# Kernel optimization log

Measured on AMD Instinct MI355X. Metric: run time of the kernel, lower is better.

Reference implementation:

```python
import jax, jax.numpy as jnp
import numpy as np

B, TI, TO = 32, 128, 64
VI, VO = 32000, 32000
E, H, A = 256, 512, 512
EOS, BOS = 0, 1


def setup_inputs() -> dict:
    key = jax.random.key(0)
    ks = jax.random.split(key, 24)
    def p(k, shape):
        return jax.random.normal(k, shape, jnp.float32) * 0.05
    return {
        "inp": jax.random.randint(ks[0], (B, TI), 0, VI),
        "out": jax.random.randint(ks[1], (B, TO), 0, VO),
        "emb_inp": p(ks[2], (VI, E)),
        "emb_out": p(ks[3], (VO, E)),
        "enc_Wih_f": p(ks[4], (3 * H, E)),
        "enc_Whh_f": p(ks[5], (3 * H, H)),
        "enc_bih_f": p(ks[6], (3 * H,)),
        "enc_bhh_f": p(ks[7], (3 * H,)),
        "enc_Wih_b": p(ks[8], (3 * H, E)),
        "enc_Whh_b": p(ks[9], (3 * H, H)),
        "enc_bih_b": p(ks[10], (3 * H,)),
        "enc_bhh_b": p(ks[11], (3 * H,)),
        "dec_start_W": p(ks[12], (H, 2 * H)),
        "dec_start_b": p(ks[13], (H,)),
        "dec_Wih": p(ks[14], (3 * H, E + 2 * H)),
        "dec_Whh": p(ks[15], (3 * H, H)),
        "dec_bih": p(ks[16], (3 * H,)),
        "dec_bhh": p(ks[17], (3 * H,)),
        "attn_Wenc": p(ks[18], (A, 2 * H)),
        "attn_benc": p(ks[19], (A,)),
        "attn_Wdec": p(ks[20], (A, H)),
        "attn_bdec": p(ks[21], (A,)),
        "attn_v": p(ks[22], (A,)),
        "attn_vb": jnp.zeros((), jnp.float32),
        "logits_W": p(ks[23], (VO, 3 * H)),
        "logits_b": jnp.zeros((VO,), jnp.float32),
    }


def _gru_dir(x, Wih, bih, Whh, bhh, reverse):
    # x: [B,T,E]; precompute input projections once: [B,T,3H]
    xp = jnp.einsum('bte,ge->btg', x, Wih) + bih
    Hd = Whh.shape[1]
    def step(h, xt):
        gh = h @ Whh.T + bhh
        xr, xz, xn = jnp.split(xt, 3, -1)
        hr, hz, hn = jnp.split(gh, 3, -1)
        r = jax.nn.sigmoid(xr + hr)
        z = jax.nn.sigmoid(xz + hz)
        n = jnp.tanh(xn + r * hn)
        h_new = (1.0 - z) * n + z * h
        return h_new, h_new
    h0 = jnp.zeros((x.shape[0], Hd), x.dtype)
    _, hs = jax.lax.scan(step, h0, jnp.swapaxes(xp, 0, 1), reverse=reverse)
    return jnp.swapaxes(hs, 0, 1)  # [B,T,H]


def _forward(inp, out, emb_inp, emb_out,
             enc_Wih_f, enc_Whh_f, enc_bih_f, enc_bhh_f,
             enc_Wih_b, enc_Whh_b, enc_bih_b, enc_bhh_b,
             dec_start_W, dec_start_b, dec_Wih, dec_Whh, dec_bih, dec_bhh,
             attn_Wenc, attn_benc, attn_Wdec, attn_bdec, attn_v, attn_vb,
             logits_W, logits_b):
    x = emb_inp[inp]  # [B,TI,E]
    ef = _gru_dir(x, enc_Wih_f, enc_bih_f, enc_Whh_f, enc_bhh_f, False)
    eb = _gru_dir(x, enc_Wih_b, enc_bih_b, enc_Whh_b, enc_bhh_b, True)
    enc = jnp.concatenate([ef, eb], -1)  # [B,TI,2H]
    mask = (inp != EOS).astype(jnp.float32)
    lengths = jnp.minimum(mask.sum(1).astype(jnp.int32), TI - 1)
    last = enc[jnp.arange(enc.shape[0]), lengths]  # [B,2H]
    dec0 = last @ dec_start_W.T + dec_start_b  # [B,H]
    enc_proj = jnp.einsum('btd,ad->bta', enc, attn_Wenc) + attn_benc  # [B,TI,A]

    def attend(dec):
        dp = dec @ attn_Wdec.T + attn_bdec  # [B,A]
        s = jnp.tanh(enc_proj + dp[:, None, :]) @ attn_v + attn_vb  # [B,TI]
        s = jnp.where(mask > 0, s, -jnp.inf)
        pr = jax.nn.softmax(s, -1)
        return jnp.einsum('bt,btd->bd', pr, enc), pr

    a0, _ = attend(dec0)

    def step(carry, tok):
        h, a = carry
        e = emb_out[tok]  # [B,E]
        xg = jnp.concatenate([e, a], -1) @ dec_Wih.T + dec_bih
        hg = h @ dec_Whh.T + dec_bhh
        xr, xz, xn = jnp.split(xg, 3, -1)
        hr, hz, hn = jnp.split(hg, 3, -1)
        r = jax.nn.sigmoid(xr + hr)
        z = jax.nn.sigmoid(xz + hz)
        n = jnp.tanh(xn + r * hn)
        h_new = (1.0 - z) * n + z * h
        a_new, _ = attend(h_new)
        lg = jnp.concatenate([h_new, a_new], -1) @ logits_W.T + logits_b
        return (h_new, a_new), lg

    toks = jnp.swapaxes(out[:, :-1], 0, 1)  # [TO-1, B]
    _, lgs = jax.lax.scan(step, (dec0, a0), toks)  # [TO-1,B,VO]
    first = jnp.log(jax.nn.one_hot(jnp.full((out.shape[0],), BOS), VO) + 1e-9)
    return jnp.swapaxes(jnp.concatenate([first[None], lgs], 0), 0, 1)  # [B,TO,VO]


def reference(inp, out, emb_inp, emb_out,
              enc_Wih_f, enc_Whh_f, enc_bih_f, enc_bhh_f,
              enc_Wih_b, enc_Whh_b, enc_bih_b, enc_bhh_b,
              dec_start_W, dec_start_b, dec_Wih, dec_Whh, dec_bih, dec_bhh,
              attn_Wenc, attn_benc, attn_Wdec, attn_bdec, attn_v, attn_vb,
              logits_W, logits_b):
    return _forward(inp, out, emb_inp, emb_out,
                    enc_Wih_f, enc_Whh_f, enc_bih_f, enc_bhh_f,
                    enc_Wih_b, enc_Whh_b, enc_bih_b, enc_bhh_b,
                    dec_start_W, dec_start_b, dec_Wih, dec_Whh, dec_bih, dec_bhh,
                    attn_Wenc, attn_benc, attn_Wdec, attn_bdec, attn_v, attn_vb,
                    logits_W, logits_b)
```

## Files before the change

### kernel.cpp

```cpp
#include <hip/hip_runtime.h>
#include <math.h>
#include <stdint.h>

#define B_   32
#define TI_  128
#define TO_  64
#define E_   256
#define H_   512
#define A_   512
#define VO_  32000
#define G3_  1536
#define D2H_ 1024

using short8 = __attribute__((ext_vector_type(8))) short;
using f32x4  = __attribute__((ext_vector_type(4))) float;

__device__ __forceinline__ unsigned short f2bf(float x) {
  uint32_t u = __builtin_bit_cast(uint32_t, x);
  uint32_t r = (u + 0x7fffu + ((u >> 16) & 1u)) >> 16;
  return (unsigned short)r;
}


__global__ __launch_bounds__(256) void k_zero(float* __restrict__ p, int n) {
  int i = blockIdx.x * 256 + threadIdx.x;
  if (i < n) p[i] = 0.f;
}

__global__ __launch_bounds__(256) void k_zero_u16(unsigned short* __restrict__ p, int n) {
  int i = blockIdx.x * 256 + threadIdx.x;
  if (i < n) p[i] = 0;
}

__global__ __launch_bounds__(256) void k_cvt_bf16(const float* __restrict__ in,
                                                  unsigned short* __restrict__ out, int n8) {
  int i = blockIdx.x * 256 + threadIdx.x;
  if (i >= n8) return;
  float4 a = ((const float4*)in)[2 * i];
  float4 b = ((const float4*)in)[2 * i + 1];
  ushort4 lo = make_ushort4(f2bf(a.x), f2bf(a.y), f2bf(a.z), f2bf(a.w));
  ushort4 hi = make_ushort4(f2bf(b.x), f2bf(b.y), f2bf(b.z), f2bf(b.w));
  ((ushort4*)out)[2 * i] = lo;
  ((ushort4*)out)[2 * i + 1] = hi;
}

__global__ __launch_bounds__(256) void k_gather_x(const int* __restrict__ inp,
                                                  const float* __restrict__ emb,
                                                  float* __restrict__ x) {
  int idx = blockIdx.x * 256 + threadIdx.x;
  int total = B_ * TI_ * E_ / 4;
  if (idx >= total) return;
  int row = idx / (E_ / 4);
  int e4  = idx % (E_ / 4);
  int tok = inp[row];
  ((float4*)x)[idx] = ((const float4*)emb)[(size_t)tok * (E_ / 4) + e4];
}

__global__ __launch_bounds__(256) void k_gather_xe(const int* __restrict__ outidx,
                                                   const float* __restrict__ emb,
                                                   float* __restrict__ xe) {
  int idx = blockIdx.x * 256 + threadIdx.x;
  int total = 63 * B_ * E_ / 4;
  if (idx >= total) return;
  int row = idx / (E_ / 4);
  int e4  = idx % (E_ / 4);
  int i = row / B_, b = row % B_;
  int tok = outidx[b * TO_ + i];
  ((float4*)xe)[idx] = ((const float4*)emb)[(size_t)tok * (E_ / 4) + e4];
}

__global__ __launch_bounds__(256) void k_first(float* __restrict__ dout) {
  int idx = blockIdx.x * 256 + threadIdx.x;
  if (idx >= B_ * VO_) return;
  int b = idx / VO_, v = idx % VO_;
  dout[(size_t)b * TO_ * VO_ + v] = (v == 1) ? 0.f : -20.72326583694641f;
}


__global__ __launch_bounds__(256) void k_gemm128(
    const float* __restrict__ A, int lda,
    const float* __restrict__ W, int ldw,
    const float* __restrict__ bias,
    float* __restrict__ C, int M, int N, int K) {
  __shared__ float As[32][132];
  __shared__ float Bs[32][132];
  const int tid = threadIdx.x;
  const int m0 = blockIdx.y * 128, n0 = blockIdx.x * 128;
  const int tx = tid & 15, ty = tid >> 4;
  float acc[8][8];
#pragma unroll
  for (int i = 0; i < 8; ++i)
#pragma unroll
    for (int j = 0; j < 8; ++j) acc[i][j] = 0.f;

  for (int k0 = 0; k0 < K; k0 += 32) {
#pragma unroll
    for (int i = 0; i < 16; ++i) {
      int idx = tid + i * 256;
      int kk = idx & 31, mm = idx >> 5;
      int m = m0 + mm;
      As[kk][mm] = (m < M) ? A[(size_t)m * lda + k0 + kk] : 0.f;
      Bs[kk][mm] = W[(size_t)(n0 + mm) * ldw + k0 + kk];
    }
    __syncthreads();
#pragma unroll
    for (int kk = 0; kk < 32; ++kk) {
      float4 a0 = *(const float4*)&As[kk][ty * 8];
      float4 a1 = *(const float4*)&As[kk][ty * 8 + 4];
      float4 b0 = *(const float4*)&Bs[kk][tx * 8];
      float4 b1 = *(const float4*)&Bs[kk][tx * 8 + 4];
      float av[8] = {a0.x, a0.y, a0.z, a0.w, a1.x, a1.y, a1.z, a1.w};
      float bv[8] = {b0.x, b0.y, b0.z, b0.w, b1.x, b1.y, b1.z, b1.w};
#pragma unroll
      for (int i = 0; i < 8; ++i)
#pragma unroll
        for (int j = 0; j < 8; ++j) acc[i][j] = fmaf(av[i], bv[j], acc[i][j]);
    }
    __syncthreads();
  }

#pragma unroll
  for (int i = 0; i < 8; ++i) {
    int m = m0 + ty * 8 + i;
    if (m >= M) continue;
#pragma unroll
    for (int j = 0; j < 8; ++j) {
      int n = n0 + tx * 8 + j;
      C[(size_t)m * N + n] = acc[i][j] + bias[n];
    }
  }
}


__global__ __launch_bounds__(256) void k_logits_mfma(
    const unsigned short* __restrict__ A,
    const unsigned short* __restrict__ Bt,
    const float* __restrict__ bias,
    float* __restrict__ out) {
  __shared__ alignas(16) unsigned short As[128 * 32];
  __shared__ alignas(16) unsigned short Bs[128 * 32];
  const int tid = threadIdx.x;
  const int wave = tid >> 6, lane = tid & 63;
  const int m0 = blockIdx.y * 128, n0 = blockIdx.x * 128;
  const int wr = wave >> 1, wc = wave & 1;
  const int K = G3_;

  f32x4 acc[4][4];
#pragma unroll
  for (int i = 0; i < 4; ++i)
#pragma unroll
    for (int j = 0; j < 4; ++j) acc[i][j] = (f32x4){0.f, 0.f, 0.f, 0.f};

  const int srow = tid >> 2;
  const int sbyte = (tid & 3) * 16;
  const int fr = lane & 15;
  const int fkb = (lane >> 4) * 16;

  for (int k0 = 0; k0 < K; k0 += 32) {
#pragma unroll
    for (int rd = 0; rd < 2; ++rd) {
      int row = rd * 64 + srow;
      const char* ga = (const char*)(A + (size_t)(m0 + row) * K + k0) + sbyte;
      const char* gb = (const char*)(Bt + (size_t)(n0 + row) * K + k0) + sbyte;
      __builtin_amdgcn_global_load_lds(
          (const __attribute__((address_space(1))) uint32_t*)ga,
          (__attribute__((address_space(3))) uint32_t*)((char*)As + rd * 4096 + wave * 1024),
          16, 0, 0);
      __builtin_amdgcn_global_load_lds(
          (const __attribute__((address_space(1))) uint32_t*)gb,
          (__attribute__((address_space(3))) uint32_t*)((char*)Bs + rd * 4096 + wave * 1024),
          16, 0, 0);
    }
    __syncthreads();

    short8 af[4], bf[4];
#pragma unroll
    for (int i = 0; i < 4; ++i) {
      int ar = wr * 64 + i * 16 + fr;
      int bc = wc * 64 + i * 16 + fr;
      af[i] = *(const short8*)((const char*)As + ar * 64 + fkb);
      bf[i] = *(const short8*)((const char*)Bs + bc * 64 + fkb);
    }
#pragma unroll
    for (int i = 0; i < 4; ++i)
#pragma unroll
      for (int j = 0; j < 4; ++j)
        acc[i][j] = __builtin_amdgcn_mfma_f32_16x16x32_bf16(af[i], bf[j], acc[i][j], 0, 0, 0);
    __syncthreads();
  }

  const int crow = (lane >> 4) * 4, ccol = lane & 15;
#pragma unroll
  for (int i = 0; i < 4; ++i) {
#pragma unroll
    for (int r = 0; r < 4; ++r) {
      int m = m0 + wr * 64 + i * 16 + crow + r;
      if (m >= 63 * B_) continue;
      int b = m & 31, st = m >> 5;
      float* orow = out + ((size_t)b * TO_ + st + 1) * VO_;
#pragma unroll
      for (int j = 0; j < 4; ++j) {
        int n = n0 + wc * 64 + j * 16 + ccol;
        orow[n] = acc[i][j][r] + bias[n];
      }
    }
  }
}


__global__ __launch_bounds__(256) void k_enc_step(
    const float* __restrict__ hf_in, float* __restrict__ hf_out,
    const float* __restrict__ hb_in, float* __restrict__ hb_out,
    const float* __restrict__ xp_f, const float* __restrict__ xp_b,
    const float* __restrict__ Whh_f, const float* __restrict__ bhh_f,
    const float* __restrict__ Whh_b, const float* __restrict__ bhh_b,
    float* __restrict__ enc, int t) {
  __shared__ float hs[32 * 516];
  const int bid = blockIdx.x;
  const int dir = bid >> 6;
  const int slice = bid & 63;
  const float* h_in  = dir ? hb_in : hf_in;
  float*       h_out = dir ? hb_out : hf_out;
  const float* xp    = dir ? xp_b : xp_f;
  const float* Whh   = dir ? Whh_b : Whh_f;
  const float* bhh   = dir ? bhh_b : bhh_f;
  const int tt = dir ? (TI_ - 1 - t) : t;
  const int tid = threadIdx.x;

#pragma unroll
  for (int i = 0; i < 16; ++i) {
    int idx4 = tid + i * 256;
    int flat = idx4 * 4;
    int mm = flat >> 9, kk = flat & 511;
    *(float4*)&hs[mm * 516 + kk] = *(const float4*)(h_in + (size_t)mm * H_ + kk);
  }
  __syncthreads();

  const int m = tid & 31, c = tid >> 5;
  const int col = slice * 8 + c;
  const float* hrow = hs + m * 516;
  const float4* wr = (const float4*)(Whh + (size_t)col * H_);
  const float4* wz = (const float4*)(Whh + (size_t)(H_ + col) * H_);
  const float4* wn = (const float4*)(Whh + (size_t)(2 * H_ + col) * H_);
  float accr = 0.f, accz = 0.f, accn = 0.f;
#pragma unroll 4
  for (int k4 = 0; k4 < H_ / 4; ++k4) {
    float4 h4 = *(const float4*)(hrow + k4 * 4);
    float4 r = wr[k4], z = wz[k4], n = wn[k4];
    accr = fmaf(h4.x, r.x, fmaf(h4.y, r.y, fmaf(h4.z, r.z, fmaf(h4.w, r.w, accr))));
    accz = fmaf(h4.x, z.x, fmaf(h4.y, z.y, fmaf(h4.z, z.z, fmaf(h4.w, z.w, accz))));
    accn = fmaf(h4.x, n.x, fmaf(h4.y, n.y, fmaf(h4.z, n.z, fmaf(h4.w, n.w, accn))));
  }
  size_t xoff = ((size_t)m * TI_ + tt) * G3_ + col;
  float xr = xp[xoff], xz = xp[xoff + 512], xn = xp[xoff + 1024];
  float hr = accr + bhh[col];
  float hz = accz + bhh[512 + col];
  float hn = accn + bhh[1024 + col];
  float r = 1.f / (1.f + expf(-(xr + hr)));
  float z = 1.f / (1.f + expf(-(xz + hz)));
  float nn = tanhf(xn + r * hn);
  float hold = hrow[col];
  float hnew = (1.f - z) * nn + z * hold;
  h_out[m * H_ + col] = hnew;
  enc[((size_t)m * TI_ + tt) * D2H_ + dir * H_ + col] = hnew;
}


__global__ __launch_bounds__(256) void k_dec_step(
    const float* __restrict__ h_in, float* __restrict__ h_out,
    const float* __restrict__ a_in, const float* __restrict__ XE,
    const float* __restrict__ Wih, const float* __restrict__ Whh,
    const float* __restrict__ bhh,
    unsigned short* __restrict__ HA, int step) {
  __shared__ float buf[32 * 516];
  const int tid = threadIdx.x;
  const int m = tid & 31, c = tid >> 5;
  const int col = blockIdx.x * 8 + c;
  const float* hrow = buf + m * 516;
  float axr = 0.f, axz = 0.f, axn = 0.f, ahr = 0.f, ahz = 0.f, ahn = 0.f;

#pragma unroll
  for (int i = 0; i < 16; ++i) {
    int idx4 = tid + i * 256;
    int flat = idx4 * 4;
    int mm = flat >> 9, kk = flat & 511;
    *(float4*)&buf[mm * 516 + kk] = *(const float4*)(a_in + (size_t)mm * D2H_ + kk);
  }
  __syncthreads();
  {
    const float4* wr = (const float4*)(Wih + (size_t)col * 1280 + 256);
    const float4* wz = (const float4*)(Wih + (size_t)(512 + col) * 1280 + 256);
    const float4* wn = (const float4*)(Wih + (size_t)(1024 + col) * 1280 + 256);
#pragma unroll 4
    for (int k4 = 0; k4 < 128; ++k4) {
      float4 h4 = *(const float4*)(hrow + k4 * 4);
      float4 r = wr[k4], z = wz[k4], n = wn[k4];
      axr = fmaf(h4.x, r.x, fmaf(h4.y, r.y, fmaf(h4.z, r.z, fmaf(h4.w, r.w, axr))));
      axz = fmaf(h4.x, z.x, fmaf(h4.y, z.y, fmaf(h4.z, z.z, fmaf(h4.w, z.w, axz))));
      axn = fmaf(h4.x, n.x, fmaf(h4.y, n.y, fmaf(h4.z, n.z, fmaf(h4.w, n.w, axn))));
    }
  }
  __syncthreads();

#pragma unroll
  for (int i = 0; i < 16; ++i) {
    int idx4 = tid + i * 256;
    int flat = idx4 * 4;
    int mm = flat >> 9, kk = flat & 511;
    *(float4*)&buf[mm * 516 + kk] = *(const float4*)(a_in + (size_t)mm * D2H_ + 512 + kk);
  }
  __syncthreads();
  {
    const float4* wr = (const float4*)(Wih + (size_t)col * 1280 + 768);
    const float4* wz = (const float4*)(Wih + (size_t)(512 + col) * 1280 + 768);
    const float4* wn = (const float4*)(Wih + (size_t)(1024 + col) * 1280 + 768);
#pragma unroll 4
    for (int k4 = 0; k4 < 128; ++k4) {
      float4 h4 = *(const float4*)(hrow + k4 * 4);
      float4 r = wr[k4], z = wz[k4], n = wn[k4];
      axr = fmaf(h4.x, r.x, fmaf(h4.y, r.y, fmaf(h4.z, r.z, fmaf(h4.w, r.w, axr))));
      axz = fmaf(h4.x, z.x, fmaf(h4.y, z.y, fmaf(h4.z, z.z, fmaf(h4.w, z.w, axz))));
      axn = fmaf(h4.x, n.x, fmaf(h4.y, n.y, fmaf(h4.z, n.z, fmaf(h4.w, n.w, axn))));
    }
  }
  __syncthreads();

#pragma unroll
  for (int i = 0; i < 16; ++i) {
    int idx4 = tid + i * 256;
    int flat = idx4 * 4;
    int mm = flat >> 9, kk = flat & 511;
    *(float4*)&buf[mm * 516 + kk] = *(const float4*)(h_in + (size_t)mm * H_ + kk);
  }
  __syncthreads();
  {
    const float4* wr = (const float4*)(Whh + (size_t)col * H_);
    const float4* wz = (const float4*)(Whh + (size_t)(512 + col) * H_);
    const float4* wn = (const float4*)(Whh + (size_t)(1024 + col) * H_);
#pragma unroll 4
    for (int k4 = 0; k4 < 128; ++k4) {
      float4 h4 = *(const float4*)(hrow + k4 * 4);
      float4 r = wr[k4], z = wz[k4], n = wn[k4];
      ahr = fmaf(h4.x, r.x, fmaf(h4.y, r.y, fmaf(h4.z, r.z, fmaf(h4.w, r.w, ahr))));
      ahz = fmaf(h4.x, z.x, fmaf(h4.y, z.z, fmaf(h4.z, z.z, fmaf(h4.w, z.w, ahz))));
      ahn = fmaf(h4.x, n.x, fmaf(h4.y, n.y, fmaf(h4.z, n.z, fmaf(h4.w, n.w, ahn))));
    }
  }

  size_t xrow = ((size_t)step * B_ + m) * G3_;
  float xr = XE[xrow + col] + axr;
  float xz = XE[xrow + 512 + col] + axz;
  float xn = XE[xrow + 1024 + col] + axn;
  float hr = ahr + bhh[col];
  float hz = ahz + bhh[512 + col];
  float hn = ahn + bhh[1024 + col];
  float r = 1.f / (1.f + expf(-(xr + hr)));
  float z = 1.f / (1.f + expf(-(xz + hz)));
  float nn = tanhf(xn + r * hn);
  float hold = hrow[col];
  float hnew = (1.f - z) * nn + z * hold;
  h_out[m * H_ + col] = hnew;
  HA[xrow + col] = f2bf(hnew);
}


__global__ __launch_bounds__(256) void k_attend(
    const float* __restrict__ h_src, const float* __restrict__ enc,
    const float* __restrict__ enc_proj, const int* __restrict__ inp,
    const float* __restrict__ Wdec, const float* __restrict__ bdec,
    const float* __restrict__ v, const float* __restrict__ vb,
    float* __restrict__ a_out, unsigned short* __restrict__ HA, int step) {
  __shared__ float hq[512];
  __shared__ float dp[512];
  __shared__ float vv[512];
  __shared__ float part[256];
  __shared__ float sc[128];
  __shared__ float red[128];
  const int b = blockIdx.x, tid = threadIdx.x;

  hq[tid] = h_src[b * H_ + tid];
  hq[tid + 256] = h_src[b * H_ + 256 + tid];
  vv[tid] = v[tid];
  vv[tid + 256] = v[tid + 256];
  __syncthreads();

#pragma unroll
  for (int jj = 0; jj < 2; ++jj) {
    int j = tid + jj * 256;
    const float4* w4 = (const float4*)(Wdec + (size_t)j * H_);
    float acc = 0.f;
#pragma unroll 4
    for (int k4 = 0; k4 < H_ / 4; ++k4) {
      float4 w = w4[k4];
      float4 h4 = *(const float4*)&hq[k4 * 4];
      acc = fmaf(h4.x, w.x, fmaf(h4.y, w.y, fmaf(h4.z, w.z, fmaf(h4.w, w.w, acc))));
    }
    dp[j] = acc + bdec[j];
  }
  __syncthreads();

  {
    int t = tid & 127, half = tid >> 7;
    const float* ep = enc_proj + ((size_t)b * TI_ + t) * A_ + half * 256;
    const float* dph = dp + half * 256;
    const float* vh = vv + half * 256;
    float p = 0.f;
    for (int a = 0; a < 256; ++a) p = fmaf(vh[a], tanhf(ep[a] + dph[a]), p);
    part[tid] = p;
  }
  __syncthreads();
  if (tid < 128) {
    float s = part[tid] + part[tid + 128] + vb[0];
    if (inp[b * TI_ + tid] == 0) s = -INFINITY;
    sc[tid] = s;
    red[tid] = s;
  }
  __syncthreads();
  for (int o = 64; o > 0; o >>= 1) {
    if (tid < o) red[tid] = fmaxf(red[tid], red[tid + o]);
    __syncthreads();
  }
  float mx = red[0];
  __syncthreads();
  if (tid < 128) {
    float e = expf(sc[tid] - mx);
    sc[tid] = e;
    red[tid] = e;
  }
  __syncthreads();
  for (int o = 64; o > 0; o >>= 1) {
    if (tid < o) red[tid] += red[tid + o];
    __syncthreads();
  }
  float inv = 1.f / red[0];
  __syncthreads();

  float4 acc = make_float4(0.f, 0.f, 0.f, 0.f);
  const float4* e4p = (const float4*)(enc + (size_t)b * TI_ * D2H_) + tid;
#pragma unroll 4
  for (int t2 = 0; t2 < TI_; ++t2) {
    float pr = sc[t2] * inv;
    float4 ev = e4p[(size_t)t2 * (D2H_ / 4)];
    acc.x = fmaf(pr, ev.x, acc.x);
    acc.y = fmaf(pr, ev.y, acc.y);
    acc.z = fmaf(pr, ev.z, acc.z);
    acc.w = fmaf(pr, ev.w, acc.w);
  }
  *(float4*)(a_out + (size_t)b * D2H_ + tid * 4) = acc;
  if (step >= 0) {
    unsigned short* hp = HA + ((size_t)step * B_ + b) * G3_ + H_ + tid * 4;
    *(ushort4*)hp = make_ushort4(f2bf(acc.x), f2bf(acc.y), f2bf(acc.z), f2bf(acc.w));
  }
}


__global__ __launch_bounds__(256) void k_dec0(
    const int* __restrict__ inp, const float* __restrict__ enc,
    const float* __restrict__ Wst, const float* __restrict__ bst,
    float* __restrict__ h0) {
  __shared__ float last[1024];
  __shared__ int redi[128];
  __shared__ int slen;
  const int b = blockIdx.x, tid = threadIdx.x;
  if (tid < 128) redi[tid] = (inp[b * TI_ + tid] != 0) ? 1 : 0;
  __syncthreads();
  for (int o = 64; o > 0; o >>= 1) {
    if (tid < o) redi[tid] += redi[tid + o];
    __syncthreads();
  }
  if (tid == 0) slen = min(redi[0], TI_ - 1);
  __syncthreads();
  int len = slen;
#pragma unroll
  for (int i = 0; i < 4; ++i)
    last[tid + i * 256] = enc[((size_t)b * TI_ + len) * D2H_ + tid + i * 256];
  __syncthreads();
#pragma unroll
  for (int jj = 0; jj < 2; ++jj) {
    int j = tid + jj * 256;
    const float4* w4 = (const float4*)(Wst + (size_t)j * D2H_);
    float acc = 0.f;
#pragma unroll 4
    for (int k4 = 0; k4 < D2H_ / 4; ++k4) {
      float4 w = w4[k4];
      float4 l4 = *(const float4*)&last[k4 * 4];
      acc = fmaf(l4.x, w.x, fmaf(l4.y, w.y, fmaf(l4.z, w.z, fmaf(l4.w, w.w, acc))));
    }
    h0[b * H_ + j] = acc + bst[j];
  }
}


extern "C" void kernel_launch(void* const* d_in, const int* in_sizes, int n_in,
                              void* d_out, int out_size, void* d_ws, size_t ws_size,
                              hipStream_t stream) {
  const int*   inp     = (const int*)d_in[0];
  const int*   outi    = (const int*)d_in[1];
  const float* emb_inp = (const float*)d_in[2];
  const float* emb_out = (const float*)d_in[3];
  const float* eWih_f  = (const float*)d_in[4];
  const float* eWhh_f  = (const float*)d_in[5];
  const float* ebih_f  = (const float*)d_in[6];
  const float* ebhh_f  = (const float*)d_in[7];
  const float* eWih_b  = (const float*)d_in[8];
  const float* eWhh_b  = (const float*)d_in[9];
  const float* ebih_b  = (const float*)d_in[10];
  const float* ebhh_b  = (const float*)d_in[11];
  const float* dsW     = (const float*)d_in[12];
  const float* dsb     = (const float*)d_in[13];
  const float* dWih    = (const float*)d_in[14];
  const float* dWhh    = (const float*)d_in[15];
  const float* dbih    = (const float*)d_in[16];
  const float* dbhh    = (const float*)d_in[17];
  const float* aWenc   = (const float*)d_in[18];
  const float* abenc   = (const float*)d_in[19];
  const float* aWdec   = (const float*)d_in[20];
  const float* abdec   = (const float*)d_in[21];
  const float* av      = (const float*)d_in[22];
  const float* avb     = (const float*)d_in[23];
  const float* lW      = (const float*)d_in[24];
  const float* lb      = (const float*)d_in[25];
  float* dout = (float*)d_out;

  float* ws = (float*)d_ws;
  size_t off = 0;
  auto alloc = [&](size_t n) { float* p = ws + off; off += n; return p; };
  float* x    = alloc((size_t)B_ * TI_ * E_);
  float* xp_f = alloc((size_t)B_ * TI_ * G3_);
  float* xp_b = alloc((size_t)B_ * TI_ * G3_);
  float* enc  = alloc((size_t)B_ * TI_ * D2H_);
  float* encp = alloc((size_t)B_ * TI_ * A_);
  float* xe   = alloc((size_t)63 * B_ * E_);
  float* XE   = alloc((size_t)63 * B_ * G3_);
  unsigned short* HAb = (unsigned short*)alloc((size_t)2048 * G3_ / 2);
  unsigned short* lWb = (unsigned short*)alloc((size_t)VO_ * G3_ / 2);
  float* hf0  = alloc(B_ * H_);
  float* hf1  = alloc(B_ * H_);
  float* hb0  = alloc(B_ * H_);
  float* hb1  = alloc(B_ * H_);
  float* hd0  = alloc(B_ * H_);
  float* hd1  = alloc(B_ * H_);
  float* adec = alloc(B_ * D2H_);

  k_zero<<<(2 * B_ * H_ + 255) / 256, 256, 0, stream>>>(hf0, B_ * H_);
  k_zero<<<(2 * B_ * H_ + 255) / 256, 256, 0, stream>>>(hb0, B_ * H_);
  k_zero_u16<<<(32 * G3_) / 256, 256, 0, stream>>>(HAb + (size_t)2016 * G3_, 32 * G3_);

  k_cvt_bf16<<<((VO_ * G3_ / 8) + 255) / 256, 256, 0, stream>>>(lW, lWb, VO_ * G3_ / 8);

  k_gather_x<<<(B_ * TI_ * E_ / 4 + 255) / 256, 256, 0, stream>>>(inp, emb_inp, x);
  dim3 g1(G3_ / 128, (B_ * TI_) / 128);
  k_gemm128<<<g1, 256, 0, stream>>>(x, E_, eWih_f, E_, ebih_f, xp_f, B_ * TI_, G3_, E_);
  k_gemm128<<<g1, 256, 0, stream>>>(x, E_, eWih_b, E_, ebih_b, xp_b, B_ * TI_, G3_, E_);

  float* hfb[2] = {hf0, hf1};
  float* hbb[2] = {hb0, hb1};
  for (int t = 0; t < TI_; ++t) {
    k_enc_step<<<128, 256, 0, stream>>>(hfb[t & 1], hfb[(t + 1) & 1],
                                        hbb[t & 1], hbb[(t + 1) & 1],
                                        xp_f, xp_b, eWhh_f, ebhh_f, eWhh_b, ebhh_b,
                                        enc, t);
  }

  dim3 g2(A_ / 128, (B_ * TI_) / 128);
  k_gemm128<<<g2, 256, 0, stream>>>(enc, D2H_, aWenc, D2H_, abenc, encp, B_ * TI_, A_, D2H_);

  k_dec0<<<B_, 256, 0, stream>>>(inp, enc, dsW, dsb, hd0);
  k_attend<<<B_, 256, 0, stream>>>(hd0, enc, encp, inp, aWdec, abdec, av, avb, adec, HAb, -1);

  k_gather_xe<<<(63 * B_ * E_ / 4 + 255) / 256, 256, 0, stream>>>(outi, emb_out, xe);
  dim3 g3(G3_ / 128, (63 * B_ + 127) / 128);
  k_gemm128<<<g3, 256, 0, stream>>>(xe, E_, dWih, E_ + D2H_, dbih, XE, 63 * B_, G3_, E_);

  float* hdb[2] = {hd0, hd1};
  for (int i = 0; i < 63; ++i) {
    k_dec_step<<<64, 256, 0, stream>>>(hdb[i & 1], hdb[(i + 1) & 1], adec, XE,
                                       dWih, dWhh, dbhh, HAb, i);
    k_attend<<<B_, 256, 0, stream>>>(hdb[(i + 1) & 1], enc, encp, inp,
                                     aWdec, abdec, av, avb, adec, HAb, i);
  }

  dim3 g4(VO_ / 128, 16);
  k_logits_mfma<<<g4, 256, 0, stream>>>(HAb, lWb, lb, dout);

  k_first<<<(B_ * VO_ + 255) / 256, 256, 0, stream>>>(dout);
}
```

Baseline: 10.89 ms.

## Fuse encoder and decoder step loops into persistent kernels with grid barriers

Replaces the 128 per-timestep encoder launches with one persistent 128-block kernel, and the 127 decoder-step and attend launches with one persistent 64-block kernel. Steps inside each kernel are separated by a software grid barrier built from an atomic counter. This removes per-launch overhead and launch gaps on the serial recurrence. In exchange, every block must be co-resident and the spin barrier carries its own latency. The encoder also gains a redundant tanh expression that is computed and then overwritten.

```diff
diff --git a/kernel.cpp b/kernel.cpp
--- a/kernel.cpp
+++ b/kernel.cpp
@@ -21,15 +21,26 @@
   return (unsigned short)r;
 }
 
-
-__global__ __launch_bounds__(256) void k_zero(float* __restrict__ p, int n) {
+__device__ __forceinline__ void gbar(int* bar, int target) {
+  __syncthreads();
+  if (threadIdx.x == 0) {
+    __threadfence();
+    atomicAdd(bar, 1);
+    while (__hip_atomic_load(bar, __ATOMIC_RELAXED, __HIP_MEMORY_SCOPE_AGENT) < target)
+      __builtin_amdgcn_s_sleep(4);
+    __threadfence();
+  }
+  __syncthreads();
+}
+
+__global__ __launch_bounds__(256) void k_init(float* __restrict__ hf0,
+                                              float* __restrict__ hb0,
+                                              unsigned short* __restrict__ HAtail,
+                                              int* __restrict__ bar) {
   int i = blockIdx.x * 256 + threadIdx.x;
-  if (i < n) p[i] = 0.f;
-}
-
-__global__ __launch_bounds__(256) void k_zero_u16(unsigned short* __restrict__ p, int n) {
-  int i = blockIdx.x * 256 + threadIdx.x;
-  if (i < n) p[i] = 0;
+  if (i < B_ * H_) { hf0[i] = 0.f; hb0[i] = 0.f; }
+  if (i < 32 * G3_) HAtail[i] = 0;
+  if (i < 2) bar[i] = 0;
 }
 
 __global__ __launch_bounds__(256) void k_cvt_bf16(const float* __restrict__ in,
@@ -38,10 +49,8 @@
   if (i >= n8) return;
   float4 a = ((const float4*)in)[2 * i];
   float4 b = ((const float4*)in)[2 * i + 1];
-  ushort4 lo = make_ushort4(f2bf(a.x), f2bf(a.y), f2bf(a.z), f2bf(a.w));
-  ushort4 hi = make_ushort4(f2bf(b.x), f2bf(b.y), f2bf(b.z), f2bf(b.w));
-  ((ushort4*)out)[2 * i] = lo;
-  ((ushort4*)out)[2 * i + 1] = hi;
+  ((ushort4*)out)[2 * i]     = make_ushort4(f2bf(a.x), f2bf(a.y), f2bf(a.z), f2bf(a.w));
+  ((ushort4*)out)[2 * i + 1] = make_ushort4(f2bf(b.x), f2bf(b.y), f2bf(b.z), f2bf(b.w));
 }
 
 __global__ __launch_bounds__(256) void k_gather_x(const int* __restrict__ inp,
@@ -76,7 +85,6 @@
   dout[(size_t)b * TO_ * VO_ + v] = (v == 1) ? 0.f : -20.72326583694641f;
 }
 
-
 __global__ __launch_bounds__(256) void k_gemm128(
     const float* __restrict__ A, int lda,
     const float* __restrict__ W, int ldw,
@@ -130,7 +138,6 @@
     }
   }
 }
-
 
 __global__ __launch_bounds__(256) void k_logits_mfma(
     const unsigned short* __restrict__ A,
@@ -208,176 +215,75 @@
 }
 
 
-__global__ __launch_bounds__(256) void k_enc_step(
-    const float* __restrict__ hf_in, float* __restrict__ hf_out,
-    const float* __restrict__ hb_in, float* __restrict__ hb_out,
+__global__ __launch_bounds__(256) void k_encoder(
     const float* __restrict__ xp_f, const float* __restrict__ xp_b,
     const float* __restrict__ Whh_f, const float* __restrict__ bhh_f,
     const float* __restrict__ Whh_b, const float* __restrict__ bhh_b,
-    float* __restrict__ enc, int t) {
+    float* __restrict__ hf0, float* __restrict__ hf1,
+    float* __restrict__ hb0, float* __restrict__ hb1,
+    float* __restrict__ enc, int* __restrict__ bar) {
   __shared__ float hs[32 * 516];
   const int bid = blockIdx.x;
-  const int dir = bid >> 6;
-  const int slice = bid & 63;
-  const float* h_in  = dir ? hb_in : hf_in;
-  float*       h_out = dir ? hb_out : hf_out;
-  const float* xp    = dir ? xp_b : xp_f;
-  const float* Whh   = dir ? Whh_b : Whh_f;
-  const float* bhh   = dir ? bhh_b : bhh_f;
-  const int tt = dir ? (TI_ - 1 - t) : t;
+  const int dir = bid >> 6, slice = bid & 63;
+  const float* xp  = dir ? xp_b : xp_f;
+  const float* Whh = dir ? Whh_b : Whh_f;
+  const float* bhh = dir ? bhh_b : bhh_f;
+  float* hp0 = dir ? hb0 : hf0;
+  float* hp1 = dir ? hb1 : hf1;
   const int tid = threadIdx.x;
-
-#pragma unroll
-  for (int i = 0; i < 16; ++i) {
-    int idx4 = tid + i * 256;
-    int flat = idx4 * 4;
-    int mm = flat >> 9, kk = flat & 511;
-    *(float4*)&hs[mm * 516 + kk] = *(const float4*)(h_in + (size_t)mm * H_ + kk);
-  }
-  __syncthreads();
-
   const int m = tid & 31, c = tid >> 5;
   const int col = slice * 8 + c;
   const float* hrow = hs + m * 516;
   const float4* wr = (const float4*)(Whh + (size_t)col * H_);
   const float4* wz = (const float4*)(Whh + (size_t)(H_ + col) * H_);
   const float4* wn = (const float4*)(Whh + (size_t)(2 * H_ + col) * H_);
-  float accr = 0.f, accz = 0.f, accn = 0.f;
-#pragma unroll 4
-  for (int k4 = 0; k4 < H_ / 4; ++k4) {
-    float4 h4 = *(const float4*)(hrow + k4 * 4);
-    float4 r = wr[k4], z = wz[k4], n = wn[k4];
-    accr = fmaf(h4.x, r.x, fmaf(h4.y, r.y, fmaf(h4.z, r.z, fmaf(h4.w, r.w, accr))));
-    accz = fmaf(h4.x, z.x, fmaf(h4.y, z.y, fmaf(h4.z, z.z, fmaf(h4.w, z.w, accz))));
-    accn = fmaf(h4.x, n.x, fmaf(h4.y, n.y, fmaf(h4.z, n.z, fmaf(h4.w, n.w, accn))));
-  }
-  size_t xoff = ((size_t)m * TI_ + tt) * G3_ + col;
-  float xr = xp[xoff], xz = xp[xoff + 512], xn = xp[xoff + 1024];
-  float hr = accr + bhh[col];
-  float hz = accz + bhh[512 + col];
-  float hn = accn + bhh[1024 + col];
-  float r = 1.f / (1.f + expf(-(xr + hr)));
-  float z = 1.f / (1.f + expf(-(xz + hz)));
-  float nn = tanhf(xn + r * hn);
-  float hold = hrow[col];
-  float hnew = (1.f - z) * nn + z * hold;
-  h_out[m * H_ + col] = hnew;
-  enc[((size_t)m * TI_ + tt) * D2H_ + dir * H_ + col] = hnew;
-}
-
-
-__global__ __launch_bounds__(256) void k_dec_step(
-    const float* __restrict__ h_in, float* __restrict__ h_out,
-    const float* __restrict__ a_in, const float* __restrict__ XE,
-    const float* __restrict__ Wih, const float* __restrict__ Whh,
-    const float* __restrict__ bhh,
-    unsigned short* __restrict__ HA, int step) {
-  __shared__ float buf[32 * 516];
-  const int tid = threadIdx.x;
-  const int m = tid & 31, c = tid >> 5;
-  const int col = blockIdx.x * 8 + c;
-  const float* hrow = buf + m * 516;
-  float axr = 0.f, axz = 0.f, axn = 0.f, ahr = 0.f, ahz = 0.f, ahn = 0.f;
-
-#pragma unroll
-  for (int i = 0; i < 16; ++i) {
-    int idx4 = tid + i * 256;
-    int flat = idx4 * 4;
-    int mm = flat >> 9, kk = flat & 511;
-    *(float4*)&buf[mm * 516 + kk] = *(const float4*)(a_in + (size_t)mm * D2H_ + kk);
-  }
-  __syncthreads();
-  {
-    const float4* wr = (const float4*)(Wih + (size_t)col * 1280 + 256);
-    const float4* wz = (const float4*)(Wih + (size_t)(512 + col) * 1280 + 256);
-    const float4* wn = (const float4*)(Wih + (size_t)(1024 + col) * 1280 + 256);
-#pragma unroll 4
-    for (int k4 = 0; k4 < 128; ++k4) {
+  const float br = bhh[col], bz = bhh[512 + col], bn = bhh[1024 + col];
+
+  for (int t = 0; t < TI_; ++t) {
+    const float* h_in = (t & 1) ? hp1 : hp0;
+    float*       h_out = (t & 1) ? hp0 : hp1;
+    const int tt = dir ? (TI_ - 1 - t) : t;
+
+#pragma unroll
+    for (int i = 0; i < 16; ++i) {
+      int flat = (tid + i * 256) * 4;
+      int mm = flat >> 9, kk = flat & 511;
+      *(float4*)&hs[mm * 516 + kk] = *(const float4*)(h_in + (size_t)mm * H_ + kk);
+    }
+    __syncthreads();
+
+    float accr = 0.f, accz = 0.f, accn = 0.f;
+#pragma unroll 4
+    for (int k4 = 0; k4 < H_ / 4; ++k4) {
       float4 h4 = *(const float4*)(hrow + k4 * 4);
       float4 r = wr[k4], z = wz[k4], n = wn[k4];
-      axr = fmaf(h4.x, r.x, fmaf(h4.y, r.y, fmaf(h4.z, r.z, fmaf(h4.w, r.w, axr))));
-      axz = fmaf(h4.x, z.x, fmaf(h4.y, z.y, fmaf(h4.z, z.z, fmaf(h4.w, z.w, axz))));
-      axn = fmaf(h4.x, n.x, fmaf(h4.y, n.y, fmaf(h4.z, n.z, fmaf(h4.w, n.w, axn))));
-    }
-  }
-  __syncthreads();
-
-#pragma unroll
-  for (int i = 0; i < 16; ++i) {
-    int idx4 = tid + i * 256;
-    int flat = idx4 * 4;
-    int mm = flat >> 9, kk = flat & 511;
-    *(float4*)&buf[mm * 516 + kk] = *(const float4*)(a_in + (size_t)mm * D2H_ + 512 + kk);
-  }
-  __syncthreads();
-  {
-    const float4* wr = (const float4*)(Wih + (size_t)col * 1280 + 768);
-    const float4* wz = (const float4*)(Wih + (size_t)(512 + col) * 1280 + 768);
-    const float4* wn = (const float4*)(Wih + (size_t)(1024 + col) * 1280 + 768);
-#pragma unroll 4
-    for (int k4 = 0; k4 < 128; ++k4) {
-      float4 h4 = *(const float4*)(hrow + k4 * 4);
-      float4 r = wr[k4], z = wz[k4], n = wn[k4];
-      axr = fmaf(h4.x, r.x, fmaf(h4.y, r.y, fmaf(h4.z, r.z, fmaf(h4.w, r.w, axr))));
-      axz = fmaf(h4.x, z.x, fmaf(h4.y, z.y, fmaf(h4.z, z.z, fmaf(h4.w, z.w, axz))));
-      axn = fmaf(h4.x, n.x, fmaf(h4.y, n.y, fmaf(h4.z, n.z, fmaf(h4.w, n.w, axn))));
-    }
-  }
-  __syncthreads();
-
-#pragma unroll
-  for (int i = 0; i < 16; ++i) {
-    int idx4 = tid + i * 256;
-    int flat = idx4 * 4;
-    int mm = flat >> 9, kk = flat & 511;
-    *(float4*)&buf[mm * 516 + kk] = *(const float4*)(h_in + (size_t)mm * H_ + kk);
-  }
-  __syncthreads();
-  {
-    const float4* wr = (const float4*)(Whh + (size_t)col * H_);
-    const float4* wz = (const float4*)(Whh + (size_t)(512 + col) * H_);
-    const float4* wn = (const float4*)(Whh + (size_t)(1024 + col) * H_);
-#pragma unroll 4
-    for (int k4 = 0; k4 < 128; ++k4) {
-      float4 h4 = *(const float4*)(hrow + k4 * 4);
-      float4 r = wr[k4], z = wz[k4], n = wn[k4];
-      ahr = fmaf(h4.x, r.x, fmaf(h4.y, r.y, fmaf(h4.z, r.z, fmaf(h4.w, r.w, ahr))));
-      ahz = fmaf(h4.x, z.x, fmaf(h4.y, z.z, fmaf(h4.z, z.z, fmaf(h4.w, z.w, ahz))));
-      ahn = fmaf(h4.x, n.x, fmaf(h4.y, n.y, fmaf(h4.z, n.z, fmaf(h4.w, n.w, ahn))));
-    }
-  }
-
-  size_t xrow = ((size_t)step * B_ + m) * G3_;
-  float xr = XE[xrow + col] + axr;
-  float xz = XE[xrow + 512 + col] + axz;
-  float xn = XE[xrow + 1024 + col] + axn;
-  float hr = ahr + bhh[col];
-  float hz = ahz + bhh[512 + col];
-  float hn = ahn + bhh[1024 + col];
-  float r = 1.f / (1.f + expf(-(xr + hr)));
-  float z = 1.f / (1.f + expf(-(xz + hz)));
-  float nn = tanhf(xn + r * hn);
-  float hold = hrow[col];
-  float hnew = (1.f - z) * nn + z * hold;
-  h_out[m * H_ + col] = hnew;
-  HA[xrow + col] = f2bf(hnew);
-}
-
-
-__global__ __launch_bounds__(256) void k_attend(
-    const float* __restrict__ h_src, const float* __restrict__ enc,
-    const float* __restrict__ enc_proj, const int* __restrict__ inp,
-    const float* __restrict__ Wdec, const float* __restrict__ bdec,
-    const float* __restrict__ v, const float* __restrict__ vb,
-    float* __restrict__ a_out, unsigned short* __restrict__ HA, int step) {
-  __shared__ float hq[512];
-  __shared__ float dp[512];
-  __shared__ float vv[512];
-  __shared__ float part[256];
-  __shared__ float sc[128];
-  __shared__ float red[128];
-  const int b = blockIdx.x, tid = threadIdx.x;
-
+      accr = fmaf(h4.x, r.x, fmaf(h4.y, r.y, fmaf(h4.z, r.z, fmaf(h4.w, r.w, accr))));
+      accz = fmaf(h4.x, z.x, fmaf(h4.y, z.y, fmaf(h4.z, z.z, fmaf(h4.w, z.w, accz))));
+      accn = fmaf(h4.x, n.x, fmaf(h4.y, n.y, fmaf(h4.z, n.z, fmaf(h4.w, n.w, accn))));
+    }
+    size_t xoff = ((size_t)m * TI_ + tt) * G3_ + col;
+    float xr = xp[xoff], xz = xp[xoff + 512], xn = xp[xoff + 1024];
+    float r = 1.f / (1.f + expf(-(xr + accr + br)));
+    float z = 1.f / (1.f + expf(-(xz + accz + bz)));
+    float nn = tanhf(xn + accn + bn + r * 0.f + r * (accn * 0.f) + r * 0.f + (accn + bn) * 0.f + r * ((accn + bn) - (accn + bn)) + r * (accn + bn) - r * (accn + bn));
+    nn = tanhf(xn + r * (accn + bn));
+    float hold = hrow[col];
+    float hnew = (1.f - z) * nn + z * hold;
+    h_out[m * H_ + col] = hnew;
+    enc[((size_t)m * TI_ + tt) * D2H_ + dir * H_ + col] = hnew;
+
+    if (t < TI_ - 1) gbar(bar, 128 * (t + 1));
+  }
+}
+
+
+__device__ void attend_body(int b, int tid,
+                            const float* __restrict__ h_src, const float* __restrict__ enc,
+                            const float* __restrict__ encp, const int* __restrict__ inp,
+                            const float* __restrict__ Wdec, const float* __restrict__ bdec,
+                            const float* __restrict__ v, const float* __restrict__ vb,
+                            float* __restrict__ a_out, unsigned short* __restrict__ HA, int step,
+                            float* hq, float* dp, float* vv, float* part, float* sc, float* red) {
   hq[tid] = h_src[b * H_ + tid];
   hq[tid + 256] = h_src[b * H_ + 256 + tid];
   vv[tid] = v[tid];
@@ -401,7 +307,7 @@
 
   {
     int t = tid & 127, half = tid >> 7;
-    const float* ep = enc_proj + ((size_t)b * TI_ + t) * A_ + half * 256;
+    const float* ep = encp + ((size_t)b * TI_ + t) * A_ + half * 256;
     const float* dph = dp + half * 256;
     const float* vh = vv + half * 256;
     float p = 0.f;
@@ -453,40 +359,159 @@
   }
 }
 
-
-__global__ __launch_bounds__(256) void k_dec0(
+__device__ void dec_step_body(int bid, int tid,
+                              const float* __restrict__ h_in, float* __restrict__ h_out,
+                              const float* __restrict__ a_in, const float* __restrict__ XE,
+                              const float* __restrict__ Wih, const float* __restrict__ Whh,
+                              const float* __restrict__ bhh,
+                              unsigned short* __restrict__ HA, int step, float* buf) {
+  const int m = tid & 31, c = tid >> 5;
+  const int col = bid * 8 + c;
+  const float* hrow = buf + m * 516;
+  float axr = 0.f, axz = 0.f, axn = 0.f, ahr = 0.f, ahz = 0.f, ahn = 0.f;
+
+#pragma unroll
+  for (int i = 0; i < 16; ++i) {
+    int flat = (tid + i * 256) * 4;
+    int mm = flat >> 9, kk = flat & 511;
+    *(float4*)&buf[mm * 516 + kk] = *(const float4*)(a_in + (size_t)mm * D2H_ + kk);
+  }
+  __syncthreads();
+  {
+    const float4* wr = (const float4*)(Wih + (size_t)col * 1280 + 256);
+    const float4* wz = (const float4*)(Wih + (size_t)(512 + col) * 1280 + 256);
+    const float4* wn = (const float4*)(Wih + (size_t)(1024 + col) * 1280 + 256);
+#pragma unroll 4
+    for (int k4 = 0; k4 < 128; ++k4) {
+      float4 h4 = *(const float4*)(hrow + k4 * 4);
+      float4 r = wr[k4], z = wz[k4], n = wn[k4];
+      axr = fmaf(h4.x, r.x, fmaf(h4.y, r.y, fmaf(h4.z, r.z, fmaf(h4.w, r.w, axr))));
+      axz = fmaf(h4.x, z.x, fmaf(h4.y, z.y, fmaf(h4.z, z.z, fmaf(h4.w, z.w, axz))));
+      axn = fmaf(h4.x, n.x, fmaf(h4.y, n.y, fmaf(h4.z, n.z, fmaf(h4.w, n.w, axn))));
+    }
+  }
+  __syncthreads();
+
+#pragma unroll
+  for (int i = 0; i < 16; ++i) {
+    int flat = (tid + i * 256) * 4;
+    int mm = flat >> 9, kk = flat & 511;
+    *(float4*)&buf[mm * 516 + kk] = *(const float4*)(a_in + (size_t)mm * D2H_ + 512 + kk);
+  }
+  __syncthreads();
+  {
+    const float4* wr = (const float4*)(Wih + (size_t)col * 1280 + 768);
+    const float4* wz = (const float4*)(Wih + (size_t)(512 + col) * 1280 + 768);
+    const float4* wn = (const float4*)(Wih + (size_t)(1024 + col) * 1280 + 768);
+#pragma unroll 4
+    for (int k4 = 0; k4 < 128; ++k4) {
+      float4 h4 = *(const float4*)(hrow + k4 * 4);
+      float4 r = wr[k4], z = wz[k4], n = wn[k4];
+      axr = fmaf(h4.x, r.x, fmaf(h4.y, r.y, fmaf(h4.z, r.z, fmaf(h4.w, r.w, axr))));
+      axz = fmaf(h4.x, z.x, fmaf(h4.y, z.y, fmaf(h4.z, z.z, fmaf(h4.w, z.w, axz))));
+      axn = fmaf(h4.x, n.x, fmaf(h4.y, n.y, fmaf(h4.z, n.z, fmaf(h4.w, n.w, axn))));
+    }
+  }
+  __syncthreads();
+
+#pragma unroll
+  for (int i = 0; i < 16; ++i) {
+    int flat = (tid + i * 256) * 4;
+    int mm = flat >> 9, kk = flat & 511;
+    *(float4*)&buf[mm * 516 + kk] = *(const float4*)(h_in + (size_t)mm * H_ + kk);
+  }
+  __syncthreads();
+  {
+    const float4* wr = (const float4*)(Whh + (size_t)col * H_);
+    const float4* wz = (const float4*)(Whh + (size_t)(512 + col) * H_);
+    const float4* wn = (const float4*)(Whh + (size_t)(1024 + col) * H_);
+#pragma unroll 4
+    for (int k4 = 0; k4 < 128; ++k4) {
+      float4 h4 = *(const float4*)(hrow + k4 * 4);
+      float4 r = wr[k4], z = wz[k4], n = wn[k4];
+      ahr = fmaf(h4.x, r.x, fmaf(h4.y, r.y, fmaf(h4.z, r.z, fmaf(h4.w, r.w, ahr))));
+      ahz = fmaf(h4.x, z.x, fmaf(h4.y, z.y, fmaf(h4.z, z.z, fmaf(h4.w, z.w, ahz))));
+      ahn = fmaf(h4.x, n.x, fmaf(h4.y, n.y, fmaf(h4.z, n.z, fmaf(h4.w, n.w, ahn))));
+    }
+  }
+
+  size_t xrow = ((size_t)step * B_ + m) * G3_;
+  float xr = XE[xrow + col] + axr;
+  float xz = XE[xrow + 512 + col] + axz;
+  float xn = XE[xrow + 1024 + col] + axn;
+  float r = 1.f / (1.f + expf(-(xr + ahr + bhh[col])));
+  float z = 1.f / (1.f + expf(-(xz + ahz + bhh[512 + col])));
+  float nn = tanhf(xn + r * (ahn + bhh[1024 + col]));
+  float hold = hrow[col];
+  float hnew = (1.f - z) * nn + z * hold;
+  h_out[m * H_ + col] = hnew;
+  HA[xrow + col] = f2bf(hnew);
+}
+
+
+__global__ __launch_bounds__(256) void k_decoder(
     const int* __restrict__ inp, const float* __restrict__ enc,
-    const float* __restrict__ Wst, const float* __restrict__ bst,
-    float* __restrict__ h0) {
-  __shared__ float last[1024];
+    const float* __restrict__ encp,
+    const float* __restrict__ dsW, const float* __restrict__ dsb,
+    const float* __restrict__ XE, const float* __restrict__ dWih,
+    const float* __restrict__ dWhh, const float* __restrict__ dbhh,
+    const float* __restrict__ aWdec, const float* __restrict__ abdec,
+    const float* __restrict__ av, const float* __restrict__ avb,
+    float* __restrict__ hd0, float* __restrict__ hd1,
+    float* __restrict__ adec, unsigned short* __restrict__ HAb,
+    int* __restrict__ bar) {
+  __shared__ float buf[32 * 516];
+  __shared__ float hq[512], dp[512], vv[512], part[256], sc[128], red[128];
   __shared__ int redi[128];
   __shared__ int slen;
-  const int b = blockIdx.x, tid = threadIdx.x;
-  if (tid < 128) redi[tid] = (inp[b * TI_ + tid] != 0) ? 1 : 0;
-  __syncthreads();
-  for (int o = 64; o > 0; o >>= 1) {
-    if (tid < o) redi[tid] += redi[tid + o];
-    __syncthreads();
-  }
-  if (tid == 0) slen = min(redi[0], TI_ - 1);
-  __syncthreads();
-  int len = slen;
-#pragma unroll
-  for (int i = 0; i < 4; ++i)
-    last[tid + i * 256] = enc[((size_t)b * TI_ + len) * D2H_ + tid + i * 256];
-  __syncthreads();
-#pragma unroll
-  for (int jj = 0; jj < 2; ++jj) {
-    int j = tid + jj * 256;
-    const float4* w4 = (const float4*)(Wst + (size_t)j * D2H_);
-    float acc = 0.f;
-#pragma unroll 4
-    for (int k4 = 0; k4 < D2H_ / 4; ++k4) {
-      float4 w = w4[k4];
-      float4 l4 = *(const float4*)&last[k4 * 4];
-      acc = fmaf(l4.x, w.x, fmaf(l4.y, w.y, fmaf(l4.z, w.z, fmaf(l4.w, w.w, acc))));
-    }
-    h0[b * H_ + j] = acc + bst[j];
+  const int bid = blockIdx.x, tid = threadIdx.x;
+  int nsync = 0;
+
+  if (bid < 32) {
+    const int b = bid;
+    if (tid < 128) redi[tid] = (inp[b * TI_ + tid] != 0) ? 1 : 0;
+    __syncthreads();
+    for (int o = 64; o > 0; o >>= 1) {
+      if (tid < o) redi[tid] += redi[tid + o];
+      __syncthreads();
+    }
+    if (tid == 0) slen = min(redi[0], TI_ - 1);
+    __syncthreads();
+    int len = slen;
+#pragma unroll
+    for (int i = 0; i < 4; ++i)
+      buf[tid + i * 256] = enc[((size_t)b * TI_ + len) * D2H_ + tid + i * 256];
+    __syncthreads();
+#pragma unroll
+    for (int jj = 0; jj < 2; ++jj) {
+      int j = tid + jj * 256;
+      const float4* w4 = (const float4*)(dsW + (size_t)j * D2H_);
+      float acc = 0.f;
+#pragma unroll 4
+      for (int k4 = 0; k4 < D2H_ / 4; ++k4) {
+        float4 w = w4[k4];
+        float4 l4 = *(const float4*)&buf[k4 * 4];
+        acc = fmaf(l4.x, w.x, fmaf(l4.y, w.y, fmaf(l4.z, w.z, fmaf(l4.w, w.w, acc))));
+      }
+      hd0[b * H_ + j] = acc + dsb[j];
+    }
+  }
+  gbar(bar, 64 * (++nsync));
+
+  if (bid < 32)
+    attend_body(bid, tid, hd0, enc, encp, inp, aWdec, abdec, av, avb,
+                adec, HAb, -1, hq, dp, vv, part, sc, red);
+  gbar(bar, 64 * (++nsync));
+
+  for (int i = 0; i < 63; ++i) {
+    const float* h_in = (i & 1) ? hd1 : hd0;
+    float*       h_out = (i & 1) ? hd0 : hd1;
+    dec_step_body(bid, tid, h_in, h_out, adec, XE, dWih, dWhh, dbhh, HAb, i, buf);
+    gbar(bar, 64 * (++nsync));
+    if (bid < 32)
+      attend_body(bid, tid, h_out, enc, encp, inp, aWdec, abdec, av, avb,
+                  adec, HAb, i, hq, dp, vv, part, sc, red);
+    if (i < 62) gbar(bar, 64 * (++nsync));
   }
 }
 
@@ -541,10 +566,9 @@
   float* hd0  = alloc(B_ * H_);
   float* hd1  = alloc(B_ * H_);
   float* adec = alloc(B_ * D2H_);
-
-  k_zero<<<(2 * B_ * H_ + 255) / 256, 256, 0, stream>>>(hf0, B_ * H_);
-  k_zero<<<(2 * B_ * H_ + 255) / 256, 256, 0, stream>>>(hb0, B_ * H_);
-  k_zero_u16<<<(32 * G3_) / 256, 256, 0, stream>>>(HAb + (size_t)2016 * G3_, 32 * G3_);
+  int*   bar  = (int*)alloc(16);
+
+  k_init<<<192, 256, 0, stream>>>(hf0, hb0, HAb + (size_t)2016 * G3_, bar);
 
   k_cvt_bf16<<<((VO_ * G3_ / 8) + 255) / 256, 256, 0, stream>>>(lW, lWb, VO_ * G3_ / 8);
 
@@ -553,32 +577,18 @@
   k_gemm128<<<g1, 256, 0, stream>>>(x, E_, eWih_f, E_, ebih_f, xp_f, B_ * TI_, G3_, E_);
   k_gemm128<<<g1, 256, 0, stream>>>(x, E_, eWih_b, E_, ebih_b, xp_b, B_ * TI_, G3_, E_);
 
-  float* hfb[2] = {hf0, hf1};
-  float* hbb[2] = {hb0, hb1};
-  for (int t = 0; t < TI_; ++t) {
-    k_enc_step<<<128, 256, 0, stream>>>(hfb[t & 1], hfb[(t + 1) & 1],
-                                        hbb[t & 1], hbb[(t + 1) & 1],
-                                        xp_f, xp_b, eWhh_f, ebhh_f, eWhh_b, ebhh_b,
-                                        enc, t);
-  }
+  k_encoder<<<128, 256, 0, stream>>>(xp_f, xp_b, eWhh_f, ebhh_f, eWhh_b, ebhh_b,
+                                     hf0, hf1, hb0, hb1, enc, bar);
 
   dim3 g2(A_ / 128, (B_ * TI_) / 128);
   k_gemm128<<<g2, 256, 0, stream>>>(enc, D2H_, aWenc, D2H_, abenc, encp, B_ * TI_, A_, D2H_);
-
-  k_dec0<<<B_, 256, 0, stream>>>(inp, enc, dsW, dsb, hd0);
-  k_attend<<<B_, 256, 0, stream>>>(hd0, enc, encp, inp, aWdec, abdec, av, avb, adec, HAb, -1);
 
   k_gather_xe<<<(63 * B_ * E_ / 4 + 255) / 256, 256, 0, stream>>>(outi, emb_out, xe);
   dim3 g3(G3_ / 128, (63 * B_ + 127) / 128);
   k_gemm128<<<g3, 256, 0, stream>>>(xe, E_, dWih, E_ + D2H_, dbih, XE, 63 * B_, G3_, E_);
 
-  float* hdb[2] = {hd0, hd1};
-  for (int i = 0; i < 63; ++i) {
-    k_dec_step<<<64, 256, 0, stream>>>(hdb[i & 1], hdb[(i + 1) & 1], adec, XE,
-                                       dWih, dWhh, dbhh, HAb, i);
-    k_attend<<<B_, 256, 0, stream>>>(hdb[(i + 1) & 1], enc, encp, inp,
-                                     aWdec, abdec, av, avb, adec, HAb, i);
-  }
+  k_decoder<<<64, 256, 0, stream>>>(inp, enc, encp, dsW, dsb, XE, dWih, dWhh, dbhh,
+                                    aWdec, abdec, av, avb, hd0, hd1, adec, HAb, bar + 1);
 
   dim3 g4(VO_ / 128, 16);
   k_logits_mfma<<<g4, 256, 0, stream>>>(HAb, lWb, lb, dout);
```

Measured after the change: 12.75 ms. +17.1%, slower.
